# Kernel optimization log

Measured on AMD Instinct MI355X. Metric: run time of the kernel, lower is better.

Reference implementation:

```python
import jax, jax.numpy as jnp
import numpy as np
from jax import lax

K = 3; KK = K * K; S = 1; P = 1; D = 1
BN_EPS = 1e-5


def setup_inputs() -> dict:
    key = jax.random.key(0)
    ks = jax.random.split(key, 4)
    B, C, H, W = 8, 128, 64, 64
    cout = 128
    # xavier-ish scales for conv weights
    def xavier(k, shape):
        fan_in = shape[1] * shape[2] * shape[3]
        fan_out = shape[0] * shape[2] * shape[3]
        limit = np.sqrt(6.0 / (fan_in + fan_out))
        return jax.random.uniform(k, shape, jnp.float32, -limit, limit)
    return {
        "x": jax.random.normal(ks[0], (B, C, H, W), jnp.float32),
        "w_off": xavier(ks[1], (2 * KK, C, K, K)),
        "b_off": jnp.zeros((2 * KK,), jnp.float32),
        "w_mod": xavier(ks[2], (KK, C, K, K)),
        "b_mod": jnp.zeros((KK,), jnp.float32),
        "w_reg": xavier(ks[3], (cout, C, K, K)),
        "b_reg": jnp.zeros((cout,), jnp.float32),
        "gamma": jnp.ones((cout,), jnp.float32),
        "beta": jnp.zeros((cout,), jnp.float32),
    }


def _conv(x, w, b):
    y = lax.conv_general_dilated(x, w, (S, S), [(P, P), (P, P)],
                                 rhs_dilation=(D, D),
                                 dimension_numbers=("NCHW", "OIHW", "NCHW"))
    return y + b[None, :, None, None]


def _deform_conv(x, offset, mask, w_reg, b_reg):
    B, C, H, W = x.shape
    Ho, Wo = offset.shape[2], offset.shape[3]
    # torchvision layout: [B, 2*KK, Ho, Wo], interleaved (dy, dx) per tap
    off = offset.reshape(B, KK, 2, Ho, Wo)
    dy, dx = off[:, :, 0], off[:, :, 1]                      # [B,KK,Ho,Wo]
    ki = jnp.arange(KK) // K
    kj = jnp.arange(KK) % K
    base_y = (jnp.arange(Ho) * S - P)[None, :, None] + (ki * D)[:, None, None]  # [KK,Ho,1]
    base_x = (jnp.arange(Wo) * S - P)[None, None, :] + (kj * D)[:, None, None]  # [KK,1,Wo]
    py = base_y[None].astype(x.dtype) + dy                   # [B,KK,Ho,Wo]
    px = base_x[None].astype(x.dtype) + dx

    y0f = jnp.floor(py); x0f = jnp.floor(px)
    ly = py - y0f; lx = px - x0f
    y0 = y0f.astype(jnp.int32); x0 = x0f.astype(jnp.int32)
    y1 = y0 + 1; x1 = x0 + 1

    def gather(iy, ix):
        valid = ((iy >= 0) & (iy < H) & (ix >= 0) & (ix < W)).astype(x.dtype)
        iyc = jnp.clip(iy, 0, H - 1)
        ixc = jnp.clip(ix, 0, W - 1)
        v = jax.vmap(lambda img, a, b: img[:, a, b])(x, iyc, ixc)  # [B,C,KK,Ho,Wo]
        return v * valid[:, None]

    val = (gather(y0, x0) * ((1 - ly) * (1 - lx))[:, None]
           + gather(y0, x1) * ((1 - ly) * lx)[:, None]
           + gather(y1, x0) * (ly * (1 - lx))[:, None]
           + gather(y1, x1) * (ly * lx)[:, None])               # [B,C,KK,Ho,Wo]

    patches = val * mask[:, None]                               # modulated samples
    wr = w_reg.reshape(w_reg.shape[0], C, KK)
    out = jnp.einsum("ock,bckhw->bohw", wr, patches)
    return out + b_reg[None, :, None, None]


def reference(x, w_off, b_off, w_mod, b_mod, w_reg, b_reg, gamma, beta):
    offset = _conv(x, w_off, b_off)
    modulator = 2.0 * jax.nn.sigmoid(_conv(x, w_mod, b_mod))
    y = _deform_conv(x, offset, modulator, w_reg, b_reg)
    # BatchNorm2d (training-mode batch statistics) + ReLU
    mu = y.mean(axis=(0, 2, 3), keepdims=True)
    var = y.var(axis=(0, 2, 3), keepdims=True)
    y = (y - mu) * lax.rsqrt(var + BN_EPS)
    y = y * gamma[None, :, None, None] + beta[None, :, None, None]
    return jax.nn.relu(y)
```

## Files before the change

kernel.cpp:

```cpp
#include <hip/hip_runtime.h>
#include <math.h>

#define H 64
#define W 64
#define C 128
#define NB 8
#define COUT 128
#define HWi 4096
#define NKC 36
#define PADu 40

typedef __attribute__((ext_vector_type(8))) short short8;
typedef __attribute__((ext_vector_type(8))) unsigned short ushort8;
typedef __attribute__((ext_vector_type(4))) unsigned short ushort4v;
typedef __attribute__((ext_vector_type(4))) float f32x4;

__device__ __forceinline__ unsigned short f2bf(float f){
    unsigned u = __float_as_uint(f);
    unsigned r = (u + 0x7FFFu + ((u >> 16) & 1u)) >> 16;
    return (unsigned short)r;
}
__device__ __forceinline__ float bf2f(unsigned short u){
    return __uint_as_float(((unsigned)u) << 16);
}

__global__ void k_pre(const float* __restrict__ x, unsigned short* __restrict__ xTp,
                      const float* __restrict__ w_reg, const float* __restrict__ w_off,
                      const float* __restrict__ w_mod, const float* __restrict__ b_off,
                      const float* __restrict__ b_mod,
                      unsigned short* __restrict__ wAv, unsigned short* __restrict__ w27A,
                      float* __restrict__ biasom, float* __restrict__ psum){
    int tid = threadIdx.x;
    if (blockIdx.x >= 528){
        int i = (blockIdx.x - 528) * 256 + tid;
        if (i < 147456){
            int kc = i >> 12, rem = i & 4095;
            int q = rem >> 10, r = (rem >> 3) & 127, j = rem & 7;
            int kk = kc * 32 + q * 8 + j, k = kk >> 7, c = kk & 127;
            wAv[i] = f2bf(w_reg[r * 1152 + c * 9 + k]);
        } else if (i < 147456 + 36864){
            int j2 = i - 147456;
            int kc = j2 >> 10, rem = j2 & 1023, m = rem >> 5, kkl = rem & 31;
            int kk = kc * 32 + kkl, k = kk >> 7, c = kk & 127;
            float v = 0.f;
            if (m < 18) v = w_off[m * 1152 + c * 9 + k];
            else if (m < 27) v = w_mod[(m - 18) * 1152 + c * 9 + k];
            w27A[j2] = f2bf(v);
        } else if (i < 147456 + 36864 + 32){
            int m = i - 147456 - 36864;
            biasom[m] = (m < 18) ? b_off[m] : (m < 27 ? b_mod[m - 18] : 0.f);
        } else if (i < 147456 + 36864 + 32 + 256){
            psum[i - 147456 - 36864 - 32] = 0.f;
        }
        return;
    }
    int bidx = blockIdx.x;
    int b = bidx / 66, hp = bidx - b * 66;
    unsigned short* row = xTp + (size_t)(b * 66 + hp) * 66 * 128;
    if (hp == 0 || hp == 65){
        ushort8 z = {0,0,0,0,0,0,0,0};
        for (int i = tid; i < 66 * 128 / 8; i += 256) ((ushort8*)row)[i] = z;
        return;
    }
    int h = hp - 1;
    __shared__ unsigned short s[64 * 136];
    int w = tid & 63, c0 = tid >> 6;
    for (int cc = 0; cc < 128; cc += 4){
        int c = cc + c0;
        s[w * 136 + c] = f2bf(x[(size_t)(b * 128 + c) * HWi + h * 64 + w]);
    }
    __syncthreads();
    if (tid < 32){
        ushort8 z = {0,0,0,0,0,0,0,0};
        int wp = (tid < 16) ? 0 : 65;
        int sg = tid & 15;
        *(ushort8*)(row + wp * 128 + sg * 8) = z;
    }
    for (int it = tid; it < 1024; it += 256){
        int w2 = it >> 4, sg = it & 15;
        *(ushort8*)(row + (w2 + 1) * 128 + sg * 8) = *(const ushort8*)(s + w2 * 136 + sg * 8);
    }
}

__global__ __launch_bounds__(256) void k_gemm27(const unsigned short* __restrict__ xTp,
        const unsigned short* __restrict__ w27A, const float* __restrict__ biasom,
        unsigned short* __restrict__ OM){
    __shared__ unsigned short sA[2][32 * PADu];
    __shared__ unsigned short sB[2][64 * PADu];
    int tid = threadIdx.x;
    int n0 = blockIdx.x * 64;
    int b = n0 >> 12, h = (n0 >> 6) & 63;
    int wv = tid >> 6, lane = tid & 63, quad = lane >> 4, l16 = lane & 15;
    int nl = tid >> 2, sg = tid & 3;
    f32x4 acc0 = {0.f,0.f,0.f,0.f}, acc1 = {0.f,0.f,0.f,0.f};

    ushort8 rA, rB;
    auto loadNext = [&](int kcn){
        int k = kcn >> 2, cb = (kcn & 3) << 5;
        int ki = k / 3, kj = k - ki * 3;
        if (tid < 128) rA = *(const ushort8*)(w27A + kcn * 1024 + tid * 8);
        int rowi = (b * 66 + h + ki) * 66 + (nl + kj);
        rB = *(const ushort8*)(xTp + (size_t)rowi * 128 + cb + sg * 8);
    };
    loadNext(0);
    for (int kc = 0; kc < NKC; kc++){
        int p = kc & 1;
        if (tid < 128) *(ushort8*)(&sA[p][(tid >> 2) * PADu + (tid & 3) * 8]) = rA;
        *(ushort8*)(&sB[p][nl * PADu + sg * 8]) = rB;
        if (kc + 1 < NKC) loadNext(kc + 1);
        __syncthreads();
        short8 bfrag = *(const short8*)(&sB[p][(wv * 16 + l16) * PADu + quad * 8]);
        short8 a0 = *(const short8*)(&sA[p][l16 * PADu + quad * 8]);
        short8 a1 = *(const short8*)(&sA[p][(16 + l16) * PADu + quad * 8]);
        acc0 = __builtin_amdgcn_mfma_f32_16x16x32_bf16(a0, bfrag, acc0, 0, 0, 0);
        acc1 = __builtin_amdgcn_mfma_f32_16x16x32_bf16(a1, bfrag, acc1, 0, 0, 0);
    }
    int n = n0 + wv * 16 + l16;
    #pragma unroll
    for (int t = 0; t < 2; t++){
        f32x4 a = t ? acc1 : acc0;
        ushort4v o;
        #pragma unroll
        for (int r = 0; r < 4; r++){
            int oc = t * 16 + quad * 4 + r;
            float v = a[r] + biasom[oc];
            if (oc >= 18) v = 2.f / (1.f + expf(-v));
            o[r] = f2bf(v);
        }
        *(ushort4v*)(OM + n * 32 + t * 16 + quad * 4) = o;
    }
}

__global__ __launch_bounds__(512, 4) void k_gemm128(const unsigned short* __restrict__ xTp,
        const unsigned short* __restrict__ OM, const unsigned short* __restrict__ wAv,
        const float* __restrict__ b_reg, unsigned short* __restrict__ ybf,
        float* __restrict__ psum){
    __shared__ char smem[49152];
    unsigned short* sA = (unsigned short*)smem;
    unsigned short* sB = (unsigned short*)(smem + 20480);
    int*   s_a0 = (int*)(smem + 30720);
    float* s_w0 = (float*)(smem + 39936);

    int tid = threadIdx.x;
    int n0 = blockIdx.x * 64;
    int b = n0 >> 12, h = (n0 >> 6) & 63;

    for (int idx = tid; idx < 576; idx += 512){
        int k = idx >> 6, px = idx & 63;
        int n = n0 + px;
        float dy = bf2f(OM[n * 32 + 2 * k]);
        float dx = bf2f(OM[n * 32 + 2 * k + 1]);
        float m  = bf2f(OM[n * 32 + 18 + k]);
        int ki = k / 3, kj = k - ki * 3;
        float py  = (float)(h - 1 + ki) + dy;
        float pxf = (float)(px - 1 + kj) + dx;
        float y0f = floorf(py), x0f = floorf(pxf);
        float ly = py - y0f, lx = pxf - x0f;
        int iy0 = (int)y0f, ix0 = (int)x0f;
        int cy0 = min(max(iy0 + 1, 0), 65), cy1 = min(max(iy0 + 2, 0), 65);
        int cx0 = min(max(ix0 + 1, 0), 65), cx1 = min(max(ix0 + 2, 0), 65);
        int rb = b * 66 * 66;
        s_a0[0 * 576 + idx] = ((rb + cy0 * 66) + cx0) * 128;
        s_a0[1 * 576 + idx] = ((rb + cy0 * 66) + cx1) * 128;
        s_a0[2 * 576 + idx] = ((rb + cy1 * 66) + cx0) * 128;
        s_a0[3 * 576 + idx] = ((rb + cy1 * 66) + cx1) * 128;
        s_w0[0 * 576 + idx] = (1.f - ly) * (1.f - lx) * m;
        s_w0[1 * 576 + idx] = (1.f - ly) * lx * m;
        s_w0[2 * 576 + idx] = ly * (1.f - lx) * m;
        s_w0[3 * 576 + idx] = ly * lx * m;
    }
    __syncthreads();

    int wv = tid >> 6, lane = tid & 63, quad = lane >> 4, l16 = lane & 15;
    int ocq = wv & 3, ng = wv >> 2;
    int rA = tid & 127, qA = tid >> 7;
    int spx = (tid & 255) >> 2, scq = tid & 3;
    bool samp = (tid < 256);

    f32x4 acc00 = {0.f,0.f,0.f,0.f}, acc01 = {0.f,0.f,0.f,0.f};
    f32x4 acc10 = {0.f,0.f,0.f,0.f}, acc11 = {0.f,0.f,0.f,0.f};

    ushort8 rW, rc0, rc1, rc2, rc3;
    float w0 = 0.f, w1 = 0.f, w2 = 0.f, w3 = 0.f;

    auto loadNext = [&](int kcn){
        rW = *(const ushort8*)(wAv + kcn * 4096 + tid * 8);
        if (samp){
            int k = kcn >> 2, cb = (kcn & 3) << 5;
            int idx = k * 64 + spx;
            int co = cb + scq * 8;
            w0 = s_w0[0 * 576 + idx]; w1 = s_w0[1 * 576 + idx];
            w2 = s_w0[2 * 576 + idx]; w3 = s_w0[3 * 576 + idx];
            rc0 = *(const ushort8*)(xTp + s_a0[0 * 576 + idx] + co);
            rc1 = *(const ushort8*)(xTp + s_a0[1 * 576 + idx] + co);
            rc2 = *(const ushort8*)(xTp + s_a0[2 * 576 + idx] + co);
            rc3 = *(const ushort8*)(xTp + s_a0[3 * 576 + idx] + co);
        }
    };
    loadNext(0);
    for (int kc = 0; kc < NKC; kc++){
        int p = kc & 1;
        *(ushort8*)(sA + p * 5120 + rA * PADu + qA * 8) = rW;
        if (samp){
            ushort8 o;
            #pragma unroll
            for (int s = 0; s < 8; s++){
                float v = w0 * bf2f(rc0[s]) + w1 * bf2f(rc1[s])
                        + w2 * bf2f(rc2[s]) + w3 * bf2f(rc3[s]);
                o[s] = f2bf(v);
            }
            *(ushort8*)(sB + p * 2560 + spx * PADu + scq * 8) = o;
        }
        if (kc + 1 < NKC) loadNext(kc + 1);
        __syncthreads();
        const unsigned short* A = sA + p * 5120;
        const unsigned short* Bn = sB + p * 2560;
        short8 a0 = *(const short8*)(A + (ocq * 32 + l16) * PADu + quad * 8);
        short8 a1 = *(const short8*)(A + (ocq * 32 + 16 + l16) * PADu + quad * 8);
        short8 b0 = *(const short8*)(Bn + (ng * 32 + l16) * PADu + quad * 8);
        short8 b1 = *(const short8*)(Bn + (ng * 32 + 16 + l16) * PADu + quad * 8);
        acc00 = __builtin_amdgcn_mfma_f32_16x16x32_bf16(a0, b0, acc00, 0, 0, 0);
        acc01 = __builtin_amdgcn_mfma_f32_16x16x32_bf16(a0, b1, acc01, 0, 0, 0);
        acc10 = __builtin_amdgcn_mfma_f32_16x16x32_bf16(a1, b0, acc10, 0, 0, 0);
        acc11 = __builtin_amdgcn_mfma_f32_16x16x32_bf16(a1, b1, acc11, 0, 0, 0);
    }

    __syncthreads();
    float* ls = (float*)smem;
    int sp0 = h * 64;
    #pragma unroll
    for (int to = 0; to < 2; to++){
        #pragma unroll
        for (int tn = 0; tn < 2; tn++){
            f32x4 a = to ? (tn ? acc11 : acc10) : (tn ? acc01 : acc00);
            int nl = ng * 32 + tn * 16 + l16;
            #pragma unroll
            for (int r = 0; r < 4; r++){
                int oc = ocq * 32 + to * 16 + quad * 4 + r;
                float v = a[r] + b_reg[oc];
                ybf[(size_t)(b * 128 + oc) * HWi + sp0 + nl] = f2bf(v);
                ls[oc * 68 + nl] = v;
            }
        }
    }
    __syncthreads();
    if (tid < 128){
        int oc = tid;
        float s = 0.f, s2 = 0.f;
        #pragma unroll 8
        for (int nl = 0; nl < 64; nl++){
            float v = ls[oc * 68 + nl];
            s += v; s2 = fmaf(v, v, s2);
        }
        atomicAdd(&psum[oc], s);
        atomicAdd(&psum[128 + oc], s2);
    }
}

__global__ void k_apply(const unsigned short* __restrict__ ybf, const float* __restrict__ psum,
                        const float* __restrict__ gamma, const float* __restrict__ beta,
                        float* __restrict__ out){
    int e8 = (blockIdx.x * 256 + threadIdx.x) * 8;
    int c = (e8 >> 12) & 127;
    ushort8 u = *(const ushort8*)(ybf + e8);
    float s = psum[c], s2 = psum[128 + c];
    float mean = s * (1.f / 32768.f);
    float var  = s2 * (1.f / 32768.f) - mean * mean;
    float rs = rsqrtf(var + 1e-5f);
    float g = gamma[c] * rs;
    float bt = beta[c] - mean * g;
    float4 lo, hi;
    lo.x = fmaxf(fmaf(bf2f(u[0]), g, bt), 0.f);
    lo.y = fmaxf(fmaf(bf2f(u[1]), g, bt), 0.f);
    lo.z = fmaxf(fmaf(bf2f(u[2]), g, bt), 0.f);
    lo.w = fmaxf(fmaf(bf2f(u[3]), g, bt), 0.f);
    hi.x = fmaxf(fmaf(bf2f(u[4]), g, bt), 0.f);
    hi.y = fmaxf(fmaf(bf2f(u[5]), g, bt), 0.f);
    hi.z = fmaxf(fmaf(bf2f(u[6]), g, bt), 0.f);
    hi.w = fmaxf(fmaf(bf2f(u[7]), g, bt), 0.f);
    *(float4*)(out + e8)     = lo;
    *(float4*)(out + e8 + 4) = hi;
}

extern "C" void kernel_launch(void* const* d_in, const int* in_sizes, int n_in,
                              void* d_out, int out_size, void* d_ws, size_t ws_size,
                              hipStream_t stream){
    const float* x     = (const float*)d_in[0];
    const float* w_off = (const float*)d_in[1];
    const float* b_off = (const float*)d_in[2];
    const float* w_mod = (const float*)d_in[3];
    const float* b_mod = (const float*)d_in[4];
    const float* w_reg = (const float*)d_in[5];
    const float* b_reg = (const float*)d_in[6];
    const float* gamma = (const float*)d_in[7];
    const float* beta  = (const float*)d_in[8];

    char* wsb = (char*)d_ws;
    unsigned short* xTp   = (unsigned short*)(wsb);
    unsigned short* OM    = (unsigned short*)(wsb + 8921088);
    unsigned short* ybf   = (unsigned short*)(wsb + 11018240);
    unsigned short* wAv   = (unsigned short*)(wsb + 19406848);
    unsigned short* w27A  = (unsigned short*)(wsb + 19701760);
    float*          biasom= (float*)(wsb + 19775488);
    float*          psum  = (float*)(wsb + 19775616);
    float* out = (float*)d_out;

    hipLaunchKernelGGL(k_pre,    dim3(1250), dim3(256), 0, stream, x, xTp, w_reg, w_off, w_mod, b_off, b_mod, wAv, w27A, biasom, psum);
    hipLaunchKernelGGL(k_gemm27, dim3(512),  dim3(256), 0, stream, xTp, w27A, biasom, OM);
    hipLaunchKernelGGL(k_gemm128,dim3(512),  dim3(512), 0, stream, xTp, OM, wAv, b_reg, ybf, psum);
    hipLaunchKernelGGL(k_apply,  dim3(2048), dim3(256), 0, stream, ybf, psum, gamma, beta, out);
}
```

Before: 147.5 us.

## Load GEMM weights directly into registers and double the K-chunk per sync

The main deformable GEMM now reads weight fragments straight from global memory into registers in MFMA layout, so it no longer stages them through shared memory. Each iteration processes a 64-channel chunk, which halves the number of barriers. All 512 threads now do the bilinear sampling with packed bf16 pairs. The transpose kernel packs channel pairs into 32-bit words, and the padding of the statistics buffer changes. In exchange, register pressure rises and each wave repeats its own global weight loads.

```diff
diff --git a/kernel.cpp b/kernel.cpp
--- a/kernel.cpp
+++ b/kernel.cpp
@@ -7,13 +7,15 @@
 #define NB 8
 #define COUT 128
 #define HWi 4096
-#define NKC 36
+#define NKC2 18
 #define PADu 40
+#define PB 72
 
 typedef __attribute__((ext_vector_type(8))) short short8;
 typedef __attribute__((ext_vector_type(8))) unsigned short ushort8;
 typedef __attribute__((ext_vector_type(4))) unsigned short ushort4v;
 typedef __attribute__((ext_vector_type(4))) float f32x4;
+typedef __attribute__((ext_vector_type(2))) float f32x2;
 
 __device__ __forceinline__ unsigned short f2bf(float f){
     unsigned u = __float_as_uint(f);
@@ -23,21 +25,29 @@
 __device__ __forceinline__ float bf2f(unsigned short u){
     return __uint_as_float(((unsigned)u) << 16);
 }
+__device__ __forceinline__ f32x2 up2(unsigned p){
+    f32x2 r;
+    r.x = __uint_as_float(p << 16);
+    r.y = __uint_as_float(p & 0xFFFF0000u);
+    return r;
+}
+__device__ __forceinline__ unsigned pk2(f32x2 v){
+    return (unsigned)f2bf(v.x) | ((unsigned)f2bf(v.y) << 16);
+}
 
 __global__ void k_pre(const float* __restrict__ x, unsigned short* __restrict__ xTp,
                       const float* __restrict__ w_reg, const float* __restrict__ w_off,
                       const float* __restrict__ w_mod, const float* __restrict__ b_off,
                       const float* __restrict__ b_mod,
-                      unsigned short* __restrict__ wAv, unsigned short* __restrict__ w27A,
+                      unsigned short* __restrict__ wA, unsigned short* __restrict__ w27A,
                       float* __restrict__ biasom, float* __restrict__ psum){
     int tid = threadIdx.x;
     if (blockIdx.x >= 528){
         int i = (blockIdx.x - 528) * 256 + tid;
         if (i < 147456){
-            int kc = i >> 12, rem = i & 4095;
-            int q = rem >> 10, r = (rem >> 3) & 127, j = rem & 7;
-            int kk = kc * 32 + q * 8 + j, k = kk >> 7, c = kk & 127;
-            wAv[i] = f2bf(w_reg[r * 1152 + c * 9 + k]);
+            int kc = i >> 12, rem = i & 4095, oc = rem >> 5, kkl = rem & 31;
+            int kk = kc * 32 + kkl, k = kk >> 7, c = kk & 127;
+            wA[i] = f2bf(w_reg[oc * 1152 + c * 9 + k]);
         } else if (i < 147456 + 36864){
             int j2 = i - 147456;
             int kc = j2 >> 10, rem = j2 & 1023, m = rem >> 5, kkl = rem & 31;
@@ -63,11 +73,14 @@
         return;
     }
     int h = hp - 1;
-    __shared__ unsigned short s[64 * 136];
-    int w = tid & 63, c0 = tid >> 6;
-    for (int cc = 0; cc < 128; cc += 4){
-        int c = cc + c0;
-        s[w * 136 + c] = f2bf(x[(size_t)(b * 128 + c) * HWi + h * 64 + w]);
+    __shared__ unsigned s2[64 * 69];
+    int w = tid & 63, cp = tid >> 6;
+    for (int cc = 0; cc < 16; cc++){
+        int c2 = cc * 4 + cp;
+        int c = c2 * 2;
+        float f0 = x[(size_t)(b * 128 + c)     * HWi + h * 64 + w];
+        float f1 = x[(size_t)(b * 128 + c + 1) * HWi + h * 64 + w];
+        s2[w * 69 + c2] = (unsigned)f2bf(f0) | ((unsigned)f2bf(f1) << 16);
     }
     __syncthreads();
     if (tid < 32){
@@ -78,7 +91,12 @@
     }
     for (int it = tid; it < 1024; it += 256){
         int w2 = it >> 4, sg = it & 15;
-        *(ushort8*)(row + (w2 + 1) * 128 + sg * 8) = *(const ushort8*)(s + w2 * 136 + sg * 8);
+        uint4 v;
+        v.x = s2[w2 * 69 + sg * 4 + 0];
+        v.y = s2[w2 * 69 + sg * 4 + 1];
+        v.z = s2[w2 * 69 + sg * 4 + 2];
+        v.w = s2[w2 * 69 + sg * 4 + 3];
+        *(uint4*)(row + (w2 + 1) * 128 + sg * 8) = v;
     }
 }
 
@@ -103,11 +121,11 @@
         rB = *(const ushort8*)(xTp + (size_t)rowi * 128 + cb + sg * 8);
     };
     loadNext(0);
-    for (int kc = 0; kc < NKC; kc++){
+    for (int kc = 0; kc < 36; kc++){
         int p = kc & 1;
         if (tid < 128) *(ushort8*)(&sA[p][(tid >> 2) * PADu + (tid & 3) * 8]) = rA;
         *(ushort8*)(&sB[p][nl * PADu + sg * 8]) = rB;
-        if (kc + 1 < NKC) loadNext(kc + 1);
+        if (kc + 1 < 36) loadNext(kc + 1);
         __syncthreads();
         short8 bfrag = *(const short8*)(&sB[p][(wv * 16 + l16) * PADu + quad * 8]);
         short8 a0 = *(const short8*)(&sA[p][l16 * PADu + quad * 8]);
@@ -132,14 +150,13 @@
 }
 
 __global__ __launch_bounds__(512, 4) void k_gemm128(const unsigned short* __restrict__ xTp,
-        const unsigned short* __restrict__ OM, const unsigned short* __restrict__ wAv,
+        const unsigned short* __restrict__ OM, const unsigned short* __restrict__ wA,
         const float* __restrict__ b_reg, unsigned short* __restrict__ ybf,
         float* __restrict__ psum){
-    __shared__ char smem[49152];
-    unsigned short* sA = (unsigned short*)smem;
-    unsigned short* sB = (unsigned short*)(smem + 20480);
-    int*   s_a0 = (int*)(smem + 30720);
-    float* s_w0 = (float*)(smem + 39936);
+    __shared__ char smem[36864];
+    unsigned short* sB = (unsigned short*)smem;
+    int*   s_a0 = (int*)(smem + 18432);
+    float* s_w0 = (float*)(smem + 27648);
 
     int tid = threadIdx.x;
     int n0 = blockIdx.x * 64;
@@ -173,56 +190,79 @@
 
     int wv = tid >> 6, lane = tid & 63, quad = lane >> 4, l16 = lane & 15;
     int ocq = wv & 3, ng = wv >> 2;
-    int rA = tid & 127, qA = tid >> 7;
-    int spx = (tid & 255) >> 2, scq = tid & 3;
-    bool samp = (tid < 256);
+    int spx = tid & 63, cg = tid >> 6;
 
     f32x4 acc00 = {0.f,0.f,0.f,0.f}, acc01 = {0.f,0.f,0.f,0.f};
     f32x4 acc10 = {0.f,0.f,0.f,0.f}, acc11 = {0.f,0.f,0.f,0.f};
 
-    ushort8 rW, rc0, rc1, rc2, rc3;
-    float w0 = 0.f, w1 = 0.f, w2 = 0.f, w3 = 0.f;
-
-    auto loadNext = [&](int kcn){
-        rW = *(const ushort8*)(wAv + kcn * 4096 + tid * 8);
-        if (samp){
-            int k = kcn >> 2, cb = (kcn & 3) << 5;
-            int idx = k * 64 + spx;
-            int co = cb + scq * 8;
-            w0 = s_w0[0 * 576 + idx]; w1 = s_w0[1 * 576 + idx];
-            w2 = s_w0[2 * 576 + idx]; w3 = s_w0[3 * 576 + idx];
-            rc0 = *(const ushort8*)(xTp + s_a0[0 * 576 + idx] + co);
-            rc1 = *(const ushort8*)(xTp + s_a0[1 * 576 + idx] + co);
-            rc2 = *(const ushort8*)(xTp + s_a0[2 * 576 + idx] + co);
-            rc3 = *(const ushort8*)(xTp + s_a0[3 * 576 + idx] + co);
-        }
+    ushort8 a00, a01, a10, a11;
+    ushort8 na00, na01, na10, na11;
+    ushort8 rc0, rc1, rc2, rc3;
+    float w0, w1, w2, w3;
+
+    auto loadA = [&](int kc2, ushort8& x00, ushort8& x01, ushort8& x10, ushort8& x11){
+        const unsigned short* b0 = wA + (kc2 * 2 + 0) * 4096 + quad * 8;
+        const unsigned short* b1 = wA + (kc2 * 2 + 1) * 4096 + quad * 8;
+        int r0 = (ocq * 32 + l16) * 32, r1 = (ocq * 32 + 16 + l16) * 32;
+        x00 = *(const ushort8*)(b0 + r0);
+        x10 = *(const ushort8*)(b0 + r1);
+        x01 = *(const ushort8*)(b1 + r0);
+        x11 = *(const ushort8*)(b1 + r1);
     };
-    loadNext(0);
-    for (int kc = 0; kc < NKC; kc++){
-        int p = kc & 1;
-        *(ushort8*)(sA + p * 5120 + rA * PADu + qA * 8) = rW;
-        if (samp){
-            ushort8 o;
+    auto loadB = [&](int kc2){
+        int k = kc2 >> 1, co = ((kc2 & 1) << 6) + cg * 8;
+        int idx = k * 64 + spx;
+        w0 = s_w0[idx]; w1 = s_w0[576 + idx]; w2 = s_w0[1152 + idx]; w3 = s_w0[1728 + idx];
+        rc0 = *(const ushort8*)(xTp + s_a0[idx] + co);
+        rc1 = *(const ushort8*)(xTp + s_a0[576 + idx] + co);
+        rc2 = *(const ushort8*)(xTp + s_a0[1152 + idx] + co);
+        rc3 = *(const ushort8*)(xTp + s_a0[1728 + idx] + co);
+    };
+
+    loadA(0, a00, a01, a10, a11);
+    loadB(0);
+
+    #pragma unroll 2
+    for (int kc2 = 0; kc2 < NKC2; kc2++){
+        int p = kc2 & 1;
+        unsigned short* sBp = sB + p * (64 * PB);
+        {
+            const unsigned* u0 = (const unsigned*)&rc0;
+            const unsigned* u1 = (const unsigned*)&rc1;
+            const unsigned* u2 = (const unsigned*)&rc2;
+            const unsigned* u3 = (const unsigned*)&rc3;
+            uint4 o;
+            unsigned* op = (unsigned*)&o;
             #pragma unroll
-            for (int s = 0; s < 8; s++){
-                float v = w0 * bf2f(rc0[s]) + w1 * bf2f(rc1[s])
-                        + w2 * bf2f(rc2[s]) + w3 * bf2f(rc3[s]);
-                o[s] = f2bf(v);
+            for (int j = 0; j < 4; j++){
+                f32x2 v = w0 * up2(u0[j]);
+                v += w1 * up2(u1[j]);
+                v += w2 * up2(u2[j]);
+                v += w3 * up2(u3[j]);
+                op[j] = pk2(v);
             }
-            *(ushort8*)(sB + p * 2560 + spx * PADu + scq * 8) = o;
-        }
-        if (kc + 1 < NKC) loadNext(kc + 1);
+            *(uint4*)(sBp + spx * PB + cg * 8) = o;
+        }
+        if (kc2 + 1 < NKC2){
+            loadA(kc2 + 1, na00, na01, na10, na11);
+            loadB(kc2 + 1);
+        }
         __syncthreads();
-        const unsigned short* A = sA + p * 5120;
-        const unsigned short* Bn = sB + p * 2560;
-        short8 a0 = *(const short8*)(A + (ocq * 32 + l16) * PADu + quad * 8);
-        short8 a1 = *(const short8*)(A + (ocq * 32 + 16 + l16) * PADu + quad * 8);
-        short8 b0 = *(const short8*)(Bn + (ng * 32 + l16) * PADu + quad * 8);
-        short8 b1 = *(const short8*)(Bn + (ng * 32 + 16 + l16) * PADu + quad * 8);
-        acc00 = __builtin_amdgcn_mfma_f32_16x16x32_bf16(a0, b0, acc00, 0, 0, 0);
-        acc01 = __builtin_amdgcn_mfma_f32_16x16x32_bf16(a0, b1, acc01, 0, 0, 0);
-        acc10 = __builtin_amdgcn_mfma_f32_16x16x32_bf16(a1, b0, acc10, 0, 0, 0);
-        acc11 = __builtin_amdgcn_mfma_f32_16x16x32_bf16(a1, b1, acc11, 0, 0, 0);
+        int rb0 = (ng * 32 + l16) * PB + quad * 8;
+        int rb1 = (ng * 32 + 16 + l16) * PB + quad * 8;
+        short8 b00 = *(const short8*)(sBp + rb0);
+        short8 b01 = *(const short8*)(sBp + rb0 + 32);
+        short8 b10 = *(const short8*)(sBp + rb1);
+        short8 b11 = *(const short8*)(sBp + rb1 + 32);
+        acc00 = __builtin_amdgcn_mfma_f32_16x16x32_bf16(a00, b00, acc00, 0, 0, 0);
+        acc00 = __builtin_amdgcn_mfma_f32_16x16x32_bf16(a01, b01, acc00, 0, 0, 0);
+        acc01 = __builtin_amdgcn_mfma_f32_16x16x32_bf16(a00, b10, acc01, 0, 0, 0);
+        acc01 = __builtin_amdgcn_mfma_f32_16x16x32_bf16(a01, b11, acc01, 0, 0, 0);
+        acc10 = __builtin_amdgcn_mfma_f32_16x16x32_bf16(a10, b00, acc10, 0, 0, 0);
+        acc10 = __builtin_amdgcn_mfma_f32_16x16x32_bf16(a11, b01, acc10, 0, 0, 0);
+        acc11 = __builtin_amdgcn_mfma_f32_16x16x32_bf16(a10, b10, acc11, 0, 0, 0);
+        acc11 = __builtin_amdgcn_mfma_f32_16x16x32_bf16(a11, b11, acc11, 0, 0, 0);
+        a00 = na00; a01 = na01; a10 = na10; a11 = na11;
     }
 
     __syncthreads();
@@ -239,7 +279,7 @@
                 int oc = ocq * 32 + to * 16 + quad * 4 + r;
                 float v = a[r] + b_reg[oc];
                 ybf[(size_t)(b * 128 + oc) * HWi + sp0 + nl] = f2bf(v);
-                ls[oc * 68 + nl] = v;
+                ls[oc * 69 + nl] = v;
             }
         }
     }
@@ -249,7 +289,7 @@
         float s = 0.f, s2 = 0.f;
         #pragma unroll 8
         for (int nl = 0; nl < 64; nl++){
-            float v = ls[oc * 68 + nl];
+            float v = ls[oc * 69 + nl];
             s += v; s2 = fmaf(v, v, s2);
         }
         atomicAdd(&psum[oc], s);
@@ -299,14 +339,14 @@
     unsigned short* xTp   = (unsigned short*)(wsb);
     unsigned short* OM    = (unsigned short*)(wsb + 8921088);
     unsigned short* ybf   = (unsigned short*)(wsb + 11018240);
-    unsigned short* wAv   = (unsigned short*)(wsb + 19406848);
+    unsigned short* wA    = (unsigned short*)(wsb + 19406848);
     unsigned short* w27A  = (unsigned short*)(wsb + 19701760);
     float*          biasom= (float*)(wsb + 19775488);
     float*          psum  = (float*)(wsb + 19775616);
     float* out = (float*)d_out;
 
-    hipLaunchKernelGGL(k_pre,    dim3(1250), dim3(256), 0, stream, x, xTp, w_reg, w_off, w_mod, b_off, b_mod, wAv, w27A, biasom, psum);
+    hipLaunchKernelGGL(k_pre,    dim3(1250), dim3(256), 0, stream, x, xTp, w_reg, w_off, w_mod, b_off, b_mod, wA, w27A, biasom, psum);
     hipLaunchKernelGGL(k_gemm27, dim3(512),  dim3(256), 0, stream, xTp, w27A, biasom, OM);
-    hipLaunchKernelGGL(k_gemm128,dim3(512),  dim3(512), 0, stream, xTp, OM, wAv, b_reg, ybf, psum);
+    hipLaunchKernelGGL(k_gemm128,dim3(512),  dim3(512), 0, stream, xTp, OM, wA, b_reg, ybf, psum);
     hipLaunchKernelGGL(k_apply,  dim3(2048), dim3(256), 0, stream, ybf, psum, gamma, beta, out);
 }
```

Result: slower. 166.9 us (+13.2%).
